# Kernel tuning notes

Hardware: AMD Instinct MI355X
Metric: run time of the kernel (lower is better)

The kernel has to match this reference:

```python
import jax, jax.numpy as jnp
import numpy as np

B, T, D, O = 8, 128, 512, 512


def setup_inputs() -> dict:
    key = jax.random.key(0)
    ks = jax.random.split(key, 10)
    w = 0.02  # small init scale, mimics GlorotNormal magnitude
    return {
        "inputs": jax.random.normal(ks[0], (B, T, D), dtype=jnp.float32),
        "Wa": jax.random.normal(ks[1], (O, O), dtype=jnp.float32) * w,
        "Ua": jax.random.normal(ks[2], (D, O), dtype=jnp.float32) * w,
        "Va": jax.random.normal(ks[3], (O, 1), dtype=jnp.float32) * w,
        "Ba": jax.random.normal(ks[4], (1, O), dtype=jnp.float32) * w,
        "Wo": jax.random.normal(ks[5], (O, 1), dtype=jnp.float32) * w,
        "Uo": jax.random.normal(ks[6], (D, O), dtype=jnp.float32) * w,
        "Co": jax.random.normal(ks[7], (D, O), dtype=jnp.float32) * w,
        "Bo": jax.random.normal(ks[8], (1, O), dtype=jnp.float32) * w,
        "emb": jax.random.normal(ks[9], (O, O), dtype=jnp.float32) * w,
    }


def reference(inputs, Wa, Ua, Va, Ba, Wo, Uo, Co, Bo, emb):
    # inputs: [B,T,D]. Precompute loop-invariant attention keys (incl. Ba).
    UaH = jnp.einsum('btd,do->bto', inputs, Ua) + Ba  # [B,T,O]
    # GRU 'prev_state' arg at step t is inputs[:, t-1, :] (t=0 -> last step).
    prev_h = jnp.roll(inputs, 1, axis=1)              # [B,T,D]
    xs = jnp.swapaxes(prev_h, 0, 1)                   # [T,B,D]
    b, o = inputs.shape[0], Wa.shape[0]

    def step(prev_pred, h_prev):
        # --- attention cell (query = sigmoid(prev_pred)) ---
        s = jax.nn.sigmoid(prev_pred)                  # [B,O]
        WaS = s @ Wa                                   # [B,O]
        e = jnp.tanh(UaH + WaS[:, None, :])            # [B,T,O]
        scores = jnp.squeeze(e @ Va, -1)               # [B,T]
        sm = jax.nn.softmax(scores, axis=1)            # softmax over timesteps
        ctx = jnp.einsum('bt,btd->bd', sm, inputs)     # [B,D]
        # --- cascaded GRU cell ---
        emb_out = jax.nn.softmax(prev_pred, axis=-1) @ emb  # [B,O]
        WoY = emb_out @ Wo                             # [B,1] (broadcasts over O)
        pred = WoY + h_prev @ Uo + ctx @ Co + Bo       # [B,O]
        return pred, pred

    init = jnp.zeros((b, o), dtype=inputs.dtype)
    _, out = jax.lax.scan(step, init, xs)              # [T,B,O]
    return jnp.swapaxes(out, 0, 1)                     # [B,T,O]
```

## Files before the change

kernel.cpp:

```cpp
#include <hip/hip_runtime.h>

#define L2E 1.44269504088896340736f


__device__ __forceinline__ float ld_agent(const float* p) {
  return __hip_atomic_load(p, __ATOMIC_RELAXED, __HIP_MEMORY_SCOPE_AGENT);
}
__device__ __forceinline__ void st_agent(float* p, float v) {
  __hip_atomic_store(p, v, __ATOMIC_RELAXED, __HIP_MEMORY_SCOPE_AGENT);
}

__global__ __launch_bounds__(256) void gemm_pre(
    const float* __restrict__ A, const float* __restrict__ Ua,
    const float* __restrict__ Uo, const float* __restrict__ Co,
    float* __restrict__ XW)
{
  __shared__ float sA[64][33];
  __shared__ float sB[32][68];
  const int r0 = blockIdx.x * 64;
  const int c0 = blockIdx.y * 64;
  const float* Wm; int cc0;
  if (c0 < 512)       { Wm = Ua; cc0 = c0; }
  else if (c0 < 1024) { Wm = Uo; cc0 = c0 - 512; }
  else                { Wm = Co; cc0 = c0 - 1024; }
  const int tid = threadIdx.x;
  const int ty4 = (tid >> 4) * 4;
  const int tx4 = (tid & 15) * 4;
  float acc[4][4] = {};
  for (int k0 = 0; k0 < 512; k0 += 32) {
    for (int t4 = tid; t4 < 512; t4 += 256) {
      int row = t4 >> 3, kq = (t4 & 7) << 2;
      float4 v = *reinterpret_cast<const float4*>(&A[(size_t)(r0 + row) * 512 + k0 + kq]);
      sA[row][kq] = v.x; sA[row][kq + 1] = v.y; sA[row][kq + 2] = v.z; sA[row][kq + 3] = v.w;
    }
    for (int t4 = tid; t4 < 512; t4 += 256) {
      int kk = t4 >> 4, cq = (t4 & 15) << 2;
      float4 v = *reinterpret_cast<const float4*>(&Wm[(size_t)(k0 + kk) * 512 + cc0 + cq]);
      sB[kk][cq] = v.x; sB[kk][cq + 1] = v.y; sB[kk][cq + 2] = v.z; sB[kk][cq + 3] = v.w;
    }
    __syncthreads();
    #pragma unroll 8
    for (int kk = 0; kk < 32; ++kk) {
      float a0 = sA[ty4 + 0][kk], a1 = sA[ty4 + 1][kk];
      float a2 = sA[ty4 + 2][kk], a3 = sA[ty4 + 3][kk];
      float4 bv = *reinterpret_cast<const float4*>(&sB[kk][tx4]);
      acc[0][0] += a0 * bv.x; acc[0][1] += a0 * bv.y; acc[0][2] += a0 * bv.z; acc[0][3] += a0 * bv.w;
      acc[1][0] += a1 * bv.x; acc[1][1] += a1 * bv.y; acc[1][2] += a1 * bv.z; acc[1][3] += a1 * bv.w;
      acc[2][0] += a2 * bv.x; acc[2][1] += a2 * bv.y; acc[2][2] += a2 * bv.z; acc[2][3] += a2 * bv.w;
      acc[3][0] += a3 * bv.x; acc[3][1] += a3 * bv.y; acc[3][2] += a3 * bv.z; acc[3][3] += a3 * bv.w;
    }
    __syncthreads();
  }
  for (int i = 0; i < 4; ++i) {
    float4 v = make_float4(acc[i][0], acc[i][1], acc[i][2], acc[i][3]);
    *reinterpret_cast<float4*>(&XW[(size_t)(r0 + ty4 + i) * 1536 + c0 + tx4]) = v;
  }
}

__global__ __launch_bounds__(512) void embwo_kernel(
    const float* __restrict__ emb, const float* __restrict__ Wo,
    float* __restrict__ gEmbWo)
{
  const int lane = threadIdx.x & 63;
  const int wv = threadIdx.x >> 6;
  const int kbase = blockIdx.x * 64 + wv * 8;
  for (int i = 0; i < 8; ++i) {
    const int k = kbase + i;
    float acc = 0.f;
    #pragma unroll
    for (int c = 0; c < 8; ++c) {
      int o = lane + 64 * c;
      acc += emb[(size_t)k * 512 + o] * Wo[o];
    }
    #pragma unroll
    for (int d = 1; d < 64; d <<= 1) acc += __shfl_xor(acc, d);
    if (lane == 0) gEmbWo[k] = acc;
  }
}

__global__ __launch_bounds__(256) void coop_scan(
    const float* __restrict__ Wa, const float* __restrict__ Va,
    const float* __restrict__ Ba, const float* __restrict__ Bo,
    const float* __restrict__ gXW, const float* __restrict__ gEmbWo,
    float* slotP, float* slotS, int* cntS, int* cntP, float* __restrict__ out)
{
  extern __shared__ float smem[];
  float* sWa   = smem;
  float* sUaHT = smem + 16384;
  float* sICo  = smem + 20512;
  float* sP1   = smem + 24608;
  float* sPred = smem + 28704;
  float* sS    = smem + 29216;
  float* sEmb  = smem + 29728;
  float* sVa   = smem + 30240;
  float* sWaS  = smem + 30272;
  float* sSm   = smem + 30304;
  float* sRedB = smem + 30432;
  float* sRed  = smem + 30688;

  const int tid = threadIdx.x;
  const int lane = tid & 63;
  const int wv = tid >> 6;
  const int b = blockIdx.x & 7;
  const int j = blockIdx.x >> 3;
  const int obase = j * 32;
  int* mycntS = cntS + b * 64;
  int* mycntP = cntP + b * 64;

  for (int idx = tid; idx < 512 * 32; idx += 256) {
    int k = idx >> 5, oo = idx & 31;
    sWa[idx] = Wa[(size_t)k * 512 + obase + oo];
  }
  for (int idx = tid; idx < 128 * 32; idx += 256) {
    int tt = idx >> 5, oo = idx & 31;
    int col = obase + oo;
    const float* rowp = gXW + (size_t)(b * 128 + tt) * 1536;
    sUaHT[oo * 129 + tt] = rowp[col] + Ba[col];
    sICo[tt * 32 + oo] = rowp[1024 + col];
    int tprev = (tt + 127) & 127;
    sP1[tt * 32 + oo] = gXW[(size_t)(b * 128 + tprev) * 1536 + 512 + col] + Bo[col];
  }
  if (tid < 32) sVa[tid] = Va[obase + tid];
  sEmb[tid] = gEmbWo[tid]; sEmb[tid + 256] = gEmbWo[tid + 256];
  sPred[tid] = 0.f; sPred[tid + 256] = 0.f;

  for (int t = 0; t < 128; ++t) {
    __syncthreads();

    float p1 = sPred[tid], p2 = sPred[tid + 256];
    sS[tid]       = 1.f / (1.f + exp2f(-p1 * L2E));
    sS[tid + 256] = 1.f / (1.f + exp2f(-p2 * L2E));
    float e1 = exp2f(p1 * L2E), e2 = exp2f(p2 * L2E);
    float Ep = e1 + e2;
    float Dp = e1 * sEmb[tid] + e2 * sEmb[tid + 256];
    #pragma unroll
    for (int d = 1; d < 64; d <<= 1) { Ep += __shfl_xor(Ep, d); Dp += __shfl_xor(Dp, d); }
    if (lane == 0) { sRed[wv] = Ep; sRed[4 + wv] = Dp; }
    __syncthreads();
    const float WoY = (sRed[4] + sRed[5] + sRed[6] + sRed[7])
                    / (sRed[0] + sRed[1] + sRed[2] + sRed[3]);

    {
      const int o = tid & 31, kg = tid >> 5, kb = kg * 64;
      float acc = 0.f;
      #pragma unroll 16
      for (int i = 0; i < 64; ++i) acc += sS[kb + i] * sWa[(kb + i) * 32 + o];
      sRedB[kg * 32 + o] = acc;
    }
    __syncthreads();
    if (tid < 32) {
      float w = 0.f;
      #pragma unroll
      for (int g = 0; g < 8; ++g) w += sRedB[g * 32 + tid];
      sWaS[tid] = w;
    }
    __syncthreads();

    {
      const int h = tid & 1, tp = tid >> 1;
      float acc = 0.f;
      #pragma unroll
      for (int i = 0; i < 16; ++i) {
        const int oo = h * 16 + i;
        float u = sUaHT[oo * 129 + tp] + sWaS[oo];
        float ex = exp2f(u * (2.f * L2E));
        acc += (1.f - 2.f / (1.f + ex)) * sVa[oo];
      }
      acc += __shfl_xor(acc, 1);
      if (h == 0) st_agent(slotS + (((t & 1) * 8 + b) * 16 + j) * 128 + tp, acc);
    }
    __syncthreads();
    if (tid == 0) {
      __hip_atomic_fetch_add(mycntS, 1, __ATOMIC_RELEASE, __HIP_MEMORY_SCOPE_AGENT);
      const int tgt = 16 * (t + 1);
      while (__hip_atomic_load(mycntS, __ATOMIC_ACQUIRE, __HIP_MEMORY_SCOPE_AGENT) < tgt) { }
    }
    __syncthreads();

    if (tid < 128) {
      const float* basep = slotS + ((t & 1) * 8 + b) * 2048 + tid;
      float sc = 0.f;
      #pragma unroll
      for (int jj = 0; jj < 16; ++jj) sc += ld_agent(basep + jj * 128);
      float ev = exp2f(sc * L2E);
      sSm[tid] = ev;
      float sv = ev;
      #pragma unroll
      for (int d = 1; d < 64; d <<= 1) sv += __shfl_xor(sv, d);
      if (lane == 0) sRed[8 + wv] = sv;
    }
    __syncthreads();
    const float rden = 1.f / (sRed[8] + sRed[9]);

    {
      const int o = tid & 31, g = tid >> 5, tb = g * 16;
      float acc = 0.f;
      #pragma unroll
      for (int i = 0; i < 16; ++i) acc += sSm[tb + i] * sICo[(tb + i) * 32 + o];
      sRedB[g * 32 + o] = acc;
    }
    __syncthreads();
    if (tid < 32) {
      float c = 0.f;
      #pragma unroll
      for (int g2 = 0; g2 < 8; ++g2) c += sRedB[g2 * 32 + tid];
      float pr = WoY + sP1[t * 32 + tid] + c * rden;
      out[(size_t)(b * 128 + t) * 512 + obase + tid] = pr;
      st_agent(slotP + ((t & 1) * 8 + b) * 512 + obase + tid, pr);
    }
    __syncthreads();
    if (tid == 0) {
      __hip_atomic_fetch_add(mycntP, 1, __ATOMIC_RELEASE, __HIP_MEMORY_SCOPE_AGENT);
      const int tgt = 16 * (t + 1);
      while (__hip_atomic_load(mycntP, __ATOMIC_ACQUIRE, __HIP_MEMORY_SCOPE_AGENT) < tgt) { }
    }
    __syncthreads();
    const float* pp = slotP + ((t & 1) * 8 + b) * 512;
    sPred[tid] = ld_agent(pp + tid);
    sPred[tid + 256] = ld_agent(pp + tid + 256);
  }
}

extern "C" void kernel_launch(void* const* d_in, const int* in_sizes, int n_in,
                              void* d_out, int out_size, void* d_ws, size_t ws_size,
                              hipStream_t stream)
{
  const float* inputs = (const float*)d_in[0];
  const float* Wa  = (const float*)d_in[1];
  const float* Ua  = (const float*)d_in[2];
  const float* Va  = (const float*)d_in[3];
  const float* Ba  = (const float*)d_in[4];
  const float* Wo  = (const float*)d_in[5];
  const float* Uo  = (const float*)d_in[6];
  const float* Co  = (const float*)d_in[7];
  const float* Bo  = (const float*)d_in[8];
  const float* emb = (const float*)d_in[9];
  float* out = (float*)d_out;

  char* ws = (char*)d_ws;
  int*   cntS   = (int*)(ws + 0);
  int*   cntP   = (int*)(ws + 2048);
  float* slotP  = (float*)(ws + 8192);
  float* slotS  = (float*)(ws + 40960);
  float* gEmbWo = (float*)(ws + 106496);
  float* gXW    = (float*)(ws + 131072);

  hipMemsetAsync(d_ws, 0, 4096, stream);

  dim3 gg(16, 24);
  gemm_pre<<<gg, 256, 0, stream>>>(inputs, Ua, Uo, Co, gXW);
  embwo_kernel<<<8, 512, 0, stream>>>(emb, Wo, gEmbWo);

  const int smem_bytes = 30704 * 4;
  hipFuncSetAttribute((const void*)coop_scan,
                      hipFuncAttributeMaxDynamicSharedMemorySize, smem_bytes);
  coop_scan<<<128, 256, smem_bytes, stream>>>(Wa, Va, Ba, Bo, gXW, gEmbWo,
                                              slotP, slotS, cntS, cntP, out);
}
```

Baseline: 1.334 ms.

## Replace atomic counter barriers with per-block flag tags polled by a wavefront

Swaps the fetch-add counter barrier for per-block release-stored step tags. Wavefront 0 polls all 16 sibling tags in parallel using __all, which avoids serialized atomic RMW contention on one counter. The prediction exchange now runs only in wavefront 0 and drops one block-wide __syncthreads. The aim is lower per-step inter-block synchronization latency in the 128-step serial scan. The risk is added memory-ordering subtlety, since correctness depends on the following loop-top barrier to publish sPred.

Measured after the change: 1.809 ms. 1.36x slower.

```diff
diff --git a/kernel.cpp b/kernel.cpp
--- a/kernel.cpp
+++ b/kernel.cpp
@@ -8,6 +8,12 @@
 }
 __device__ __forceinline__ void st_agent(float* p, float v) {
   __hip_atomic_store(p, v, __ATOMIC_RELAXED, __HIP_MEMORY_SCOPE_AGENT);
+}
+__device__ __forceinline__ int ld_tag(const int* p) {
+  return __hip_atomic_load(p, __ATOMIC_RELAXED, __HIP_MEMORY_SCOPE_AGENT);
+}
+__device__ __forceinline__ void st_tag_rel(int* p, int v) {
+  __hip_atomic_store(p, v, __ATOMIC_RELEASE, __HIP_MEMORY_SCOPE_AGENT);
 }
 
 __global__ __launch_bounds__(256) void gemm_pre(
@@ -82,7 +88,7 @@
     const float* __restrict__ Wa, const float* __restrict__ Va,
     const float* __restrict__ Ba, const float* __restrict__ Bo,
     const float* __restrict__ gXW, const float* __restrict__ gEmbWo,
-    float* slotP, float* slotS, int* cntS, int* cntP, float* __restrict__ out)
+    float* slotP, float* slotS, int* tagS, int* tagP, float* __restrict__ out)
 {
   extern __shared__ float smem[];
   float* sWa   = smem;
@@ -104,8 +110,10 @@
   const int b = blockIdx.x & 7;
   const int j = blockIdx.x >> 3;
   const int obase = j * 32;
-  int* mycntS = cntS + b * 64;
-  int* mycntP = cntP + b * 64;
+  int* myTagS = tagS + (b * 16 + j) * 16;
+  int* myTagP = tagP + (b * 16 + j) * 16;
+  const int* pollTagS = tagS + (b * 16 + (lane & 15)) * 16;
+  const int* pollTagP = tagP + (b * 16 + (lane & 15)) * 16;
 
   for (int idx = tid; idx < 512 * 32; idx += 256) {
     int k = idx >> 5, oo = idx & 31;
@@ -170,12 +178,12 @@
       if (h == 0) st_agent(slotS + (((t & 1) * 8 + b) * 16 + j) * 128 + tp, acc);
     }
     __syncthreads();
-    if (tid == 0) {
-      __hip_atomic_fetch_add(mycntS, 1, __ATOMIC_RELEASE, __HIP_MEMORY_SCOPE_AGENT);
-      const int tgt = 16 * (t + 1);
-      while (__hip_atomic_load(mycntS, __ATOMIC_ACQUIRE, __HIP_MEMORY_SCOPE_AGENT) < tgt) { }
-    }
-    __syncthreads();
+    if (tid == 0) st_tag_rel(myTagS, t + 1);
+    if (wv == 0) {
+      while (!__all(ld_tag(pollTagS) >= t + 1)) { }
+    }
+    __syncthreads();
+    __builtin_amdgcn_fence(__ATOMIC_ACQUIRE, "agent");
 
     if (tid < 128) {
       const float* basep = slotS + ((t & 1) * 8 + b) * 2048 + tid;
@@ -200,24 +208,26 @@
       sRedB[g * 32 + o] = acc;
     }
     __syncthreads();
-    if (tid < 32) {
-      float c = 0.f;
-      #pragma unroll
-      for (int g2 = 0; g2 < 8; ++g2) c += sRedB[g2 * 32 + tid];
-      float pr = WoY + sP1[t * 32 + tid] + c * rden;
-      out[(size_t)(b * 128 + t) * 512 + obase + tid] = pr;
-      st_agent(slotP + ((t & 1) * 8 + b) * 512 + obase + tid, pr);
-    }
-    __syncthreads();
-    if (tid == 0) {
-      __hip_atomic_fetch_add(mycntP, 1, __ATOMIC_RELEASE, __HIP_MEMORY_SCOPE_AGENT);
-      const int tgt = 16 * (t + 1);
-      while (__hip_atomic_load(mycntP, __ATOMIC_ACQUIRE, __HIP_MEMORY_SCOPE_AGENT) < tgt) { }
-    }
-    __syncthreads();
-    const float* pp = slotP + ((t & 1) * 8 + b) * 512;
-    sPred[tid] = ld_agent(pp + tid);
-    sPred[tid + 256] = ld_agent(pp + tid + 256);
+
+    if (wv == 0) {
+      float pr = 0.f;
+      if (tid < 32) {
+        float c = 0.f;
+        #pragma unroll
+        for (int g2 = 0; g2 < 8; ++g2) c += sRedB[g2 * 32 + tid];
+        pr = WoY + sP1[t * 32 + tid] + c * rden;
+        out[(size_t)(b * 128 + t) * 512 + obase + tid] = pr;
+      }
+      if (t < 127) {
+        if (tid < 32) st_agent(slotP + ((t & 1) * 8 + b) * 512 + obase + tid, pr);
+        if (tid == 0) st_tag_rel(myTagP, t + 1);
+        while (!__all(ld_tag(pollTagP) >= t + 1)) { }
+        __builtin_amdgcn_fence(__ATOMIC_ACQUIRE, "agent");
+        const float* pp = slotP + ((t & 1) * 8 + b) * 512;
+        #pragma unroll
+        for (int q = 0; q < 8; ++q) sPred[lane + q * 64] = ld_agent(pp + lane + q * 64);
+      }
+    }
   }
 }
 
@@ -238,14 +248,14 @@
   float* out = (float*)d_out;
 
   char* ws = (char*)d_ws;
-  int*   cntS   = (int*)(ws + 0);
-  int*   cntP   = (int*)(ws + 2048);
-  float* slotP  = (float*)(ws + 8192);
-  float* slotS  = (float*)(ws + 40960);
-  float* gEmbWo = (float*)(ws + 106496);
+  int*   tagS   = (int*)(ws + 0);
+  int*   tagP   = (int*)(ws + 8192);
+  float* slotP  = (float*)(ws + 16384);
+  float* slotS  = (float*)(ws + 49152);
+  float* gEmbWo = (float*)(ws + 114688);
   float* gXW    = (float*)(ws + 131072);
 
-  hipMemsetAsync(d_ws, 0, 4096, stream);
+  hipMemsetAsync(d_ws, 0, 16384, stream);
 
   dim3 gg(16, 24);
   gemm_pre<<<gg, 256, 0, stream>>>(inputs, Ua, Uo, Co, gXW);
@@ -255,5 +265,5 @@
   hipFuncSetAttribute((const void*)coop_scan,
                       hipFuncAttributeMaxDynamicSharedMemorySize, smem_bytes);
   coop_scan<<<128, 256, smem_bytes, stream>>>(Wa, Va, Ba, Bo, gXW, gEmbWo,
-                                              slotP, slotS, cntS, cntP, out);
-}
+                                              slotP, slotS, tagS, tagP, out);
+}
```

## Replace counter barriers with tagged 64-bit value+step slots polled per element

Applied to the files above, without the earlier changes.

Each value exchanged between blocks (partial scores and predictions) is packed into a 64-bit word together with a step tag. Consumers spin on the individual slots until the expected tag appears, instead of incrementing and spinning on shared atomic counters guarded by block-wide barriers. This removes the atomic read-modify-write round-trips, two `__syncthreads` per exchange, and the workspace memset launch. In exchange, every exchanged word doubles in size and consumers poll many addresses. Correctness relies on leftover tags from earlier runs or uninitialised workspace never matching the expected step.

Result: faster. 1.189 ms (-10.8%).

```diff
diff --git a/kernel.cpp b/kernel.cpp
--- a/kernel.cpp
+++ b/kernel.cpp
@@ -3,11 +3,14 @@
 #define L2E 1.44269504088896340736f
 
 
-__device__ __forceinline__ float ld_agent(const float* p) {
+typedef unsigned long long ull;
+
+__device__ __forceinline__ void st_pack(ull* p, float v, int tag) {
+  ull u = (((ull)(unsigned)tag) << 32) | (ull)__float_as_uint(v);
+  __hip_atomic_store(p, u, __ATOMIC_RELAXED, __HIP_MEMORY_SCOPE_AGENT);
+}
+__device__ __forceinline__ ull ld_pack(const ull* p) {
   return __hip_atomic_load(p, __ATOMIC_RELAXED, __HIP_MEMORY_SCOPE_AGENT);
-}
-__device__ __forceinline__ void st_agent(float* p, float v) {
-  __hip_atomic_store(p, v, __ATOMIC_RELAXED, __HIP_MEMORY_SCOPE_AGENT);
 }
 
 __global__ __launch_bounds__(256) void gemm_pre(
@@ -82,7 +85,7 @@
     const float* __restrict__ Wa, const float* __restrict__ Va,
     const float* __restrict__ Ba, const float* __restrict__ Bo,
     const float* __restrict__ gXW, const float* __restrict__ gEmbWo,
-    float* slotP, float* slotS, int* cntS, int* cntP, float* __restrict__ out)
+    ull* slotP64, ull* slotS64, float* __restrict__ out)
 {
   extern __shared__ float smem[];
   float* sWa   = smem;
@@ -104,8 +107,6 @@
   const int b = blockIdx.x & 7;
   const int j = blockIdx.x >> 3;
   const int obase = j * 32;
-  int* mycntS = cntS + b * 64;
-  int* mycntP = cntP + b * 64;
 
   for (int idx = tid; idx < 512 * 32; idx += 256) {
     int k = idx >> 5, oo = idx & 31;
@@ -167,21 +168,27 @@
         acc += (1.f - 2.f / (1.f + ex)) * sVa[oo];
       }
       acc += __shfl_xor(acc, 1);
-      if (h == 0) st_agent(slotS + (((t & 1) * 8 + b) * 16 + j) * 128 + tp, acc);
-    }
-    __syncthreads();
-    if (tid == 0) {
-      __hip_atomic_fetch_add(mycntS, 1, __ATOMIC_RELEASE, __HIP_MEMORY_SCOPE_AGENT);
-      const int tgt = 16 * (t + 1);
-      while (__hip_atomic_load(mycntS, __ATOMIC_ACQUIRE, __HIP_MEMORY_SCOPE_AGENT) < tgt) { }
-    }
-    __syncthreads();
+      if (h == 0)
+        st_pack(slotS64 + (((t & 1) * 8 + b) * 16 + j) * 128 + tp, acc, t + 1);
+    }
 
     if (tid < 128) {
-      const float* basep = slotS + ((t & 1) * 8 + b) * 2048 + tid;
+      const ull* basep = slotS64 + ((t & 1) * 8 + b) * 2048 + tid;
+      const unsigned want = (unsigned)(t + 1);
       float sc = 0.f;
-      #pragma unroll
-      for (int jj = 0; jj < 16; ++jj) sc += ld_agent(basep + jj * 128);
+      unsigned mask = 0xFFFFu;
+      while (mask) {
+        #pragma unroll
+        for (int jj = 0; jj < 16; ++jj) {
+          if (mask & (1u << jj)) {
+            ull v = ld_pack(basep + jj * 128);
+            if ((unsigned)(v >> 32) == want) {
+              sc += __uint_as_float((unsigned)v);
+              mask &= ~(1u << jj);
+            }
+          }
+        }
+      }
       float ev = exp2f(sc * L2E);
       sSm[tid] = ev;
       float sv = ev;
@@ -206,18 +213,21 @@
       for (int g2 = 0; g2 < 8; ++g2) c += sRedB[g2 * 32 + tid];
       float pr = WoY + sP1[t * 32 + tid] + c * rden;
       out[(size_t)(b * 128 + t) * 512 + obase + tid] = pr;
-      st_agent(slotP + ((t & 1) * 8 + b) * 512 + obase + tid, pr);
-    }
-    __syncthreads();
-    if (tid == 0) {
-      __hip_atomic_fetch_add(mycntP, 1, __ATOMIC_RELEASE, __HIP_MEMORY_SCOPE_AGENT);
-      const int tgt = 16 * (t + 1);
-      while (__hip_atomic_load(mycntP, __ATOMIC_ACQUIRE, __HIP_MEMORY_SCOPE_AGENT) < tgt) { }
-    }
-    __syncthreads();
-    const float* pp = slotP + ((t & 1) * 8 + b) * 512;
-    sPred[tid] = ld_agent(pp + tid);
-    sPred[tid + 256] = ld_agent(pp + tid + 256);
+      if (t < 127)
+        st_pack(slotP64 + ((t & 1) * 8 + b) * 512 + obase + tid, pr, t + 1);
+    }
+
+    if (t < 127) {
+      const ull* pp = slotP64 + ((t & 1) * 8 + b) * 512;
+      const unsigned want = (unsigned)(t + 1);
+      ull v0, v1; bool d0 = false, d1 = false;
+      do {
+        if (!d0) { v0 = ld_pack(pp + tid);       d0 = ((unsigned)(v0 >> 32) == want); }
+        if (!d1) { v1 = ld_pack(pp + tid + 256); d1 = ((unsigned)(v1 >> 32) == want); }
+      } while (!(d0 && d1));
+      sPred[tid]       = __uint_as_float((unsigned)v0);
+      sPred[tid + 256] = __uint_as_float((unsigned)v1);
+    }
   }
 }
 
@@ -238,14 +248,11 @@
   float* out = (float*)d_out;
 
   char* ws = (char*)d_ws;
-  int*   cntS   = (int*)(ws + 0);
-  int*   cntP   = (int*)(ws + 2048);
-  float* slotP  = (float*)(ws + 8192);
-  float* slotS  = (float*)(ws + 40960);
-  float* gEmbWo = (float*)(ws + 106496);
-  float* gXW    = (float*)(ws + 131072);
-
-  hipMemsetAsync(d_ws, 0, 4096, stream);
+  ull*   slotP64 = (ull*)(ws + 16384);
+  ull*   slotS64 = (ull*)(ws + 81920);
+  float* gEmbWo  = (float*)(ws + 344064);
+  float* gXW     = (float*)(ws + 360448);
+
 
   dim3 gg(16, 24);
   gemm_pre<<<gg, 256, 0, stream>>>(inputs, Ua, Uo, Co, gXW);
@@ -255,5 +262,5 @@
   hipFuncSetAttribute((const void*)coop_scan,
                       hipFuncAttributeMaxDynamicSharedMemorySize, smem_bytes);
   coop_scan<<<128, 256, smem_bytes, stream>>>(Wa, Va, Ba, Bo, gXW, gEmbWo,
-                                              slotP, slotS, cntS, cntP, out);
-}
+                                              slotP64, slotS64, out);
+}
```
